# Kernel optimization log

Hardware: AMD Instinct MI355X
Metric: run time of the kernel (lower is better)

The kernel has to match this reference:

```python
import jax, jax.numpy as jnp
import numpy as np

N_NODES = 8192
IN_DIM = 128
HIDDEN = 128
N_EDGES = 262144


def gcn_layer(x, W, b, src, dst, n):
    # GCNConv: h = D^{-1/2}(A+I)D^{-1/2} (x @ W) + b, with added self-loops
    h = x @ W  # [n, out]
    loop = jnp.arange(n, dtype=src.dtype)
    s = jnp.concatenate([src, loop])
    d = jnp.concatenate([dst, loop])
    deg = jax.ops.segment_sum(jnp.ones_like(s, dtype=h.dtype), d, num_segments=n)
    dinv = jax.lax.rsqrt(deg)  # deg >= 1 due to self-loops
    norm = dinv[s] * dinv[d]  # [E+n]
    msg = h[s] * norm[:, None]
    out = jax.ops.segment_sum(msg, d, num_segments=n)
    return out + b


def setup_inputs() -> dict:
    key = jax.random.key(0)
    ks = jax.random.split(key, 10)
    g = 1.0 / np.sqrt(HIDDEN)
    inp = {
        "x": jax.random.normal(ks[0], (N_NODES, IN_DIM), dtype=jnp.float32),
        "edge_index": jax.random.randint(ks[1], (2, N_EDGES), 0, N_NODES, dtype=jnp.int32),
        "W1": jax.random.normal(ks[2], (IN_DIM, HIDDEN), dtype=jnp.float32) * (1.0 / np.sqrt(IN_DIM)),
        "b1": jnp.zeros((HIDDEN,), dtype=jnp.float32),
        "W2": jax.random.normal(ks[3], (HIDDEN, HIDDEN), dtype=jnp.float32) * g,
        "b2": jnp.zeros((HIDDEN,), dtype=jnp.float32),
        "W_out": jax.random.normal(ks[4], (HIDDEN, HIDDEN), dtype=jnp.float32) * g,
        "b_out": jnp.zeros((HIDDEN,), dtype=jnp.float32),
        "W_edge": jax.random.normal(ks[5], (2 * HIDDEN,), dtype=jnp.float32) * (1.0 / np.sqrt(2 * HIDDEN)),
        "b_edge": jnp.zeros((), dtype=jnp.float32),
    }
    return inp


def reference(x, edge_index, W1, b1, W2, b2, W_out, b_out, W_edge, b_edge):
    src, dst = edge_index[0], edge_index[1]
    n = x.shape[0]
    h = jax.nn.relu(gcn_layer(x, W1, b1, src, dst, n))
    h = jax.nn.relu(gcn_layer(h, W2, b2, src, dst, n))
    h = h @ W_out + b_out  # [n, hidden]
    # edge_proj(cat(x_i, x_j)) decomposes: logits[i,j] = h_i.w_i + h_j.w_j + b
    w_i, w_j = W_edge[:HIDDEN], W_edge[HIDDEN:]
    a = h @ w_i  # [n]
    c = h @ w_j  # [n]
    edge_logits = a[:, None] + c[None, :] + b_edge  # [n, n]
    return edge_logits
```

## Files before the change

### kernel.cpp

```cpp
#include <hip/hip_runtime.h>

#define NN 8192
#define NE 262144
#define DIM 128
#define BCAP 128

typedef float f32x4 __attribute__((ext_vector_type(4)));
typedef float f32x2 __attribute__((ext_vector_type(2)));

__device__ __forceinline__ float4 f4fma(float s, float4 w, float4 acc) {
    acc.x = fmaf(s, w.x, acc.x);
    acc.y = fmaf(s, w.y, acc.y);
    acc.z = fmaf(s, w.z, acc.z);
    acc.w = fmaf(s, w.w, acc.w);
    return acc;
}
__device__ __forceinline__ float f4dot(float4 a, float4 b) {
    return fmaf(a.x, b.x, fmaf(a.y, b.y, fmaf(a.z, b.z, a.w * b.w)));
}

__global__ __launch_bounds__(256) void zero_kernel(int* __restrict__ cnt) {
    cnt[blockIdx.x * 256 + threadIdx.x] = 0;
}

__global__ __launch_bounds__(256) void fused_pre(const float* __restrict__ X,
                                                 const float* __restrict__ W,
                                                 float* __restrict__ G,
                                                 const int* __restrict__ src,
                                                 const int* __restrict__ dst,
                                                 int* __restrict__ cnt,
                                                 int* __restrict__ bucket,
                                                 const float* __restrict__ Wout,
                                                 const float* __restrict__ bout,
                                                 const float* __restrict__ we,
                                                 const float* __restrict__ bedge,
                                                 float* __restrict__ u,
                                                 float* __restrict__ v,
                                                 float* __restrict__ beta) {
    __shared__ float4 Wl[128 * 32];
    __shared__ float4 Xl[32 * 32];
    int tid = threadIdx.x;
    int bid = blockIdx.x;

    if (bid < 256) {
        int rbase = bid * 32;
        const float4* W4 = (const float4*)W;
#pragma unroll
        for (int i = 0; i < 16; ++i) Wl[i * 256 + tid] = W4[i * 256 + tid];
        const float4* X4 = (const float4*)(X + rbase * DIM);
#pragma unroll
        for (int i = 0; i < 4; ++i) Xl[i * 256 + tid] = X4[i * 256 + tid];
        __syncthreads();

        int tx = tid & 31;
        int ty = tid >> 5;
        float4 acc[4];
#pragma unroll
        for (int i = 0; i < 4; ++i) acc[i] = make_float4(0.f, 0.f, 0.f, 0.f);

        for (int k4 = 0; k4 < 32; ++k4) {
            float4 w0 = Wl[(k4 * 4 + 0) * 32 + tx];
            float4 w1 = Wl[(k4 * 4 + 1) * 32 + tx];
            float4 w2 = Wl[(k4 * 4 + 2) * 32 + tx];
            float4 w3 = Wl[(k4 * 4 + 3) * 32 + tx];
#pragma unroll
            for (int i = 0; i < 4; ++i) {
                float4 xv = Xl[(ty * 4 + i) * 32 + k4];
                acc[i] = f4fma(xv.x, w0, acc[i]);
                acc[i] = f4fma(xv.y, w1, acc[i]);
                acc[i] = f4fma(xv.z, w2, acc[i]);
                acc[i] = f4fma(xv.w, w3, acc[i]);
            }
        }
        float4* G4 = (float4*)G;
#pragma unroll
        for (int i = 0; i < 4; ++i) {
            int r = rbase + ty * 4 + i;
            G4[r * 32 + tx] = acc[i];
        }
        return;
    }
    if (bid < 1280) {
        int e = (bid - 256) * 256 + tid;
        int d = dst[e];
        int p = atomicAdd(&cnt[d], 1);
        if (p < BCAP) bucket[(d << 7) + p] = src[e];
        return;
    }
    float* red = (float*)Xl;
    int k = tid;
    if (k < DIM) {
        const float4* W4o = (const float4*)(Wout + (k << 7));
        const float4* we4 = (const float4*)we;
        float su = 0.f, sv = 0.f;
#pragma unroll
        for (int j = 0; j < 32; ++j) {
            float4 w = W4o[j];
            su += f4dot(w, we4[j]);
            sv += f4dot(w, we4[32 + j]);
        }
        u[k] = su;
        v[k] = sv;
    }
    red[k] = (k < DIM) ? bout[k] * we[k] : 0.f;
    __syncthreads();
    for (int off = 128; off >= 1; off >>= 1) {
        if (k < off) red[k] += red[k + off];
        __syncthreads();
    }
    float b0 = red[0];
    __syncthreads();
    red[k] = (k < DIM) ? bout[k] * we[DIM + k] : 0.f;
    __syncthreads();
    for (int off = 128; off >= 1; off >>= 1) {
        if (k < off) red[k] += red[k + off];
        __syncthreads();
    }
    if (k == 0) {
        beta[0] = b0 + bedge[0];
        beta[1] = red[0];
    }
}

__global__ __launch_bounds__(256) void gather_scale(const float* __restrict__ G1,
                                                    const int* __restrict__ cnt,
                                                    const int* __restrict__ bucket,
                                                    const float* __restrict__ b1,
                                                    f32x2* __restrict__ S2) {
    int node = blockIdx.x * 4 + (threadIdx.x >> 6);
    int lane = threadIdx.x & 63;
    const float2* G12 = (const float2*)G1;

    int degree = cnt[node];
    float dv = rsqrtf((float)(degree + 1));
    int deg = min(degree, BCAP);
    int i0 = __builtin_nontemporal_load(bucket + (node << 7) + lane);
    int i1 = __builtin_nontemporal_load(bucket + (node << 7) + 64 + lane);

    float2 selfv = G12[node * 64 + lane];
    float ax = selfv.x * dv, ay = selfv.y * dv;
    float px[8], py[8];
#pragma unroll
    for (int k = 0; k < 8; ++k) { px[k] = 0.f; py[k] = 0.f; }

    int d8 = deg & ~7;
    for (int e = 0; e < d8; e += 8) {
        int s[8];
#pragma unroll
        for (int k = 0; k < 8; ++k) s[k] = __shfl((e + k) >= 64 ? i1 : i0, (e + k) & 63);
#pragma unroll
        for (int k = 0; k < 8; ++k) {
            int ck = cnt[s[k]];
            float2 t = G12[s[k] * 64 + lane];
            float w = rsqrtf((float)(ck + 1));
            px[k] = fmaf(t.x, w, px[k]);
            py[k] = fmaf(t.y, w, py[k]);
        }
    }
    for (int e = d8; e < deg; ++e) {
        int s = __shfl(e >= 64 ? i1 : i0, e & 63);
        int ck = cnt[s];
        float2 t = G12[s * 64 + lane];
        float w = rsqrtf((float)(ck + 1));
        ax = fmaf(t.x, w, ax);
        ay = fmaf(t.y, w, ay);
    }
    float yx = ax + ((px[0] + px[1]) + (px[2] + px[3])) + ((px[4] + px[5]) + (px[6] + px[7]));
    float yy = ay + ((py[0] + py[1]) + (py[2] + py[3])) + ((py[4] + py[5]) + (py[6] + py[7]));

    const float2* B2 = (const float2*)b1;
    float2 bb = B2[lane];
    f32x2 o;
    o.x = fmaxf(fmaf(yx, dv, bb.x), 0.f) * dv;
    o.y = fmaxf(fmaf(yy, dv, bb.y), 0.f) * dv;
    __builtin_nontemporal_store(o, S2 + node * 64 + lane);
}

__global__ __launch_bounds__(256) void gemm_mid(const float* __restrict__ X,
                                                const float* __restrict__ W,
                                                float* __restrict__ G) {
    __shared__ float4 Wl[128 * 32];
    __shared__ float4 Xl[32 * 32];
    int tid = threadIdx.x;
    int rbase = blockIdx.x * 32;

    const float4* W4 = (const float4*)W;
#pragma unroll
    for (int i = 0; i < 16; ++i) Wl[i * 256 + tid] = W4[i * 256 + tid];
    const float4* X4 = (const float4*)(X + rbase * DIM);
#pragma unroll
    for (int i = 0; i < 4; ++i) Xl[i * 256 + tid] = X4[i * 256 + tid];
    __syncthreads();

    int tx = tid & 31;
    int ty = tid >> 5;
    float4 acc[4];
#pragma unroll
    for (int i = 0; i < 4; ++i) acc[i] = make_float4(0.f, 0.f, 0.f, 0.f);

    for (int k4 = 0; k4 < 32; ++k4) {
        float4 w0 = Wl[(k4 * 4 + 0) * 32 + tx];
        float4 w1 = Wl[(k4 * 4 + 1) * 32 + tx];
        float4 w2 = Wl[(k4 * 4 + 2) * 32 + tx];
        float4 w3 = Wl[(k4 * 4 + 3) * 32 + tx];
#pragma unroll
        for (int i = 0; i < 4; ++i) {
            float4 xv = Xl[(ty * 4 + i) * 32 + k4];
            acc[i] = f4fma(xv.x, w0, acc[i]);
            acc[i] = f4fma(xv.y, w1, acc[i]);
            acc[i] = f4fma(xv.z, w2, acc[i]);
            acc[i] = f4fma(xv.w, w3, acc[i]);
        }
    }

    float4* G4 = (float4*)G;
#pragma unroll
    for (int i = 0; i < 4; ++i) {
        int r = rbase + ty * 4 + i;
        G4[r * 32 + tx] = acc[i];
    }
}

__global__ __launch_bounds__(256) void agg_head(const float* __restrict__ G2,
                                                const int* __restrict__ cnt,
                                                const int* __restrict__ bucket,
                                                const float* __restrict__ b2,
                                                const float* __restrict__ u,
                                                const float* __restrict__ v,
                                                const float* __restrict__ beta,
                                                float* __restrict__ a,
                                                float* __restrict__ c) {
    int node = blockIdx.x * 4 + (threadIdx.x >> 6);
    int lane = threadIdx.x & 63;
    const float2* G22 = (const float2*)G2;

    int degree = cnt[node];
    float dv = rsqrtf((float)(degree + 1));
    int deg = min(degree, BCAP);
    int i0 = __builtin_nontemporal_load(bucket + (node << 7) + lane);
    int i1 = __builtin_nontemporal_load(bucket + (node << 7) + 64 + lane);

    float2 selfv = G22[node * 64 + lane];
    float ax = selfv.x, ay = selfv.y;
    float px[8], py[8];
#pragma unroll
    for (int k = 0; k < 8; ++k) { px[k] = 0.f; py[k] = 0.f; }

    int d8 = deg & ~7;
    for (int e = 0; e < d8; e += 8) {
        int s[8];
#pragma unroll
        for (int k = 0; k < 8; ++k) s[k] = __shfl((e + k) >= 64 ? i1 : i0, (e + k) & 63);
#pragma unroll
        for (int k = 0; k < 8; ++k) {
            float2 t = G22[s[k] * 64 + lane];
            px[k] += t.x;
            py[k] += t.y;
        }
    }
    for (int e = d8; e < deg; ++e) {
        int s = __shfl(e >= 64 ? i1 : i0, e & 63);
        float2 t = G22[s * 64 + lane];
        ax += t.x;
        ay += t.y;
    }
    float yx = ax + ((px[0] + px[1]) + (px[2] + px[3])) + ((px[4] + px[5]) + (px[6] + px[7]));
    float yy = ay + ((py[0] + py[1]) + (py[2] + py[3])) + ((py[4] + py[5]) + (py[6] + py[7]));

    const float2* B2 = (const float2*)b2;
    float2 bb = B2[lane];
    float h0 = fmaxf(fmaf(yx, dv, bb.x), 0.f);
    float h1 = fmaxf(fmaf(yy, dv, bb.y), 0.f);

    float2 uu = ((const float2*)u)[lane];
    float2 vv = ((const float2*)v)[lane];
    float pa = h0 * uu.x + h1 * uu.y;
    float pc = h0 * vv.x + h1 * vv.y;
#pragma unroll
    for (int off = 32; off >= 1; off >>= 1) {
        pa += __shfl_xor(pa, off);
        pc += __shfl_xor(pc, off);
    }
    if (lane == 0) {
        a[node] = pa + beta[0];
        c[node] = pc + beta[1];
    }
}

__global__ __launch_bounds__(256) void out_kernel(const float* __restrict__ a,
                                                  const float* __restrict__ c,
                                                  f32x4* __restrict__ out) {
    const f32x4* c4 = (const f32x4*)c;
    size_t base = (size_t)blockIdx.x * 1024 + threadIdx.x;
#pragma unroll
    for (int q = 0; q < 4; ++q) {
        size_t idx = base + q * 256;
        int i = (int)(idx >> 11);
        int j4 = (int)(idx & 2047);
        f32x4 r = c4[j4] + a[i];
        out[idx] = r;
    }
}

extern "C" void kernel_launch(void* const* d_in, const int* in_sizes, int n_in,
                              void* d_out, int out_size, void* d_ws, size_t ws_size,
                              hipStream_t stream) {
    const float* x    = (const float*)d_in[0];
    const int*   ei   = (const int*)d_in[1];
    const float* W1   = (const float*)d_in[2];
    const float* b1   = (const float*)d_in[3];
    const float* W2   = (const float*)d_in[4];
    const float* b2   = (const float*)d_in[5];
    const float* Wout = (const float*)d_in[6];
    const float* bout = (const float*)d_in[7];
    const float* We   = (const float*)d_in[8];
    const float* bedge= (const float*)d_in[9];
    const int* src = ei;
    const int* dst = ei + NE;

    int* cnt     = (int*)d_ws;
    int* bucket  = cnt + NN;
    float* u     = (float*)(bucket + NN * BCAP);
    float* v     = u + DIM;
    float* beta  = v + DIM;
    float* g1    = beta + 16;
    float* s2    = g1 + NN * DIM;
    float* g2    = s2 + NN * DIM;
    float* av    = g2 + NN * DIM;
    float* cv    = av + NN;

    float* out = (float*)d_out;

    zero_kernel<<<32, 256, 0, stream>>>(cnt);
    fused_pre<<<1281, 256, 0, stream>>>(x, W1, g1, src, dst, cnt, bucket,
                                        Wout, bout, We, bedge, u, v, beta);
    gather_scale<<<NN / 4, 256, 0, stream>>>(g1, cnt, bucket, b1, (f32x2*)s2);
    gemm_mid<<<NN / 32, 256, 0, stream>>>(s2, W2, g2);
    agg_head<<<NN / 4, 256, 0, stream>>>(g2, cnt, bucket, b2, u, v, beta, av, cv);
    out_kernel<<<(NN * NN / 4) / 1024, 256, 0, stream>>>(av, cv, (f32x4*)out);
}
```

Measured before the change: 110.0 us.

## Build edge buckets with chunked LDS histograms, scan, and deterministic placement

Replaces global-atomic bucket construction with a three-phase counting sort. Each of 64 chunks builds a per-destination histogram in shared memory, a scan kernel computes per-chunk offsets, and a place kernel scatters source indices using LDS atomics. The aim is to remove contention on global atomics and the separate zero kernel. In exchange it adds two kernel launches, a 64x8192 histogram round-trip through memory, and place_kernel runs only 64 blocks, which limits parallelism.

```diff
diff --git a/kernel.cpp b/kernel.cpp
--- a/kernel.cpp
+++ b/kernel.cpp
@@ -4,6 +4,8 @@
 #define NE 262144
 #define DIM 128
 #define BCAP 128
+#define NCH 64
+#define CHE (NE / NCH)
 
 typedef float f32x4 __attribute__((ext_vector_type(4)));
 typedef float f32x2 __attribute__((ext_vector_type(2)));
@@ -19,17 +21,11 @@
     return fmaf(a.x, b.x, fmaf(a.y, b.y, fmaf(a.z, b.z, a.w * b.w)));
 }
 
-__global__ __launch_bounds__(256) void zero_kernel(int* __restrict__ cnt) {
-    cnt[blockIdx.x * 256 + threadIdx.x] = 0;
-}
-
 __global__ __launch_bounds__(256) void fused_pre(const float* __restrict__ X,
                                                  const float* __restrict__ W,
                                                  float* __restrict__ G,
-                                                 const int* __restrict__ src,
                                                  const int* __restrict__ dst,
-                                                 int* __restrict__ cnt,
-                                                 int* __restrict__ bucket,
+                                                 int* __restrict__ hist,
                                                  const float* __restrict__ Wout,
                                                  const float* __restrict__ bout,
                                                  const float* __restrict__ we,
@@ -37,8 +33,10 @@
                                                  float* __restrict__ u,
                                                  float* __restrict__ v,
                                                  float* __restrict__ beta) {
-    __shared__ float4 Wl[128 * 32];
-    __shared__ float4 Xl[32 * 32];
+    __shared__ char smem[80 * 1024] __attribute__((aligned(16)));
+    float4* Wl = (float4*)smem;
+    float4* Xl = (float4*)(smem + 64 * 1024);
+    int* histL = (int*)smem;
     int tid = threadIdx.x;
     int bid = blockIdx.x;
 
@@ -80,11 +78,17 @@
         }
         return;
     }
-    if (bid < 1280) {
-        int e = (bid - 256) * 256 + tid;
-        int d = dst[e];
-        int p = atomicAdd(&cnt[d], 1);
-        if (p < BCAP) bucket[(d << 7) + p] = src[e];
+    if (bid < 256 + NCH) {
+        int c = bid - 256;
+        for (int i = tid; i < NN; i += 256) histL[i] = 0;
+        __syncthreads();
+        const int* dch = dst + c * CHE;
+        for (int i = tid; i < CHE; i += 256) {
+            atomicAdd(&histL[dch[i]], 1);
+        }
+        __syncthreads();
+        int* hc = hist + c * NN;
+        for (int i = tid; i < NN; i += 256) hc[i] = histL[i];
         return;
     }
     float* red = (float*)Xl;
@@ -119,6 +123,39 @@
     if (k == 0) {
         beta[0] = b0 + bedge[0];
         beta[1] = red[0];
+    }
+}
+
+__global__ __launch_bounds__(256) void scan_kernel(const int* __restrict__ hist,
+                                                   int* __restrict__ offs,
+                                                   int* __restrict__ cnt) {
+    int n = blockIdx.x * 256 + threadIdx.x;
+    int run = n << 7;
+#pragma unroll
+    for (int c = 0; c < NCH; ++c) {
+        int t = hist[c * NN + n];
+        offs[c * NN + n] = run;
+        run += t;
+    }
+    cnt[n] = run - (n << 7);
+}
+
+__global__ __launch_bounds__(256) void place_kernel(const int* __restrict__ src,
+                                                    const int* __restrict__ dst,
+                                                    const int* __restrict__ offs,
+                                                    int* __restrict__ bucket) {
+    __shared__ int cur[NN];
+    int tid = threadIdx.x;
+    int c = blockIdx.x;
+    const int* oc = offs + c * NN;
+    for (int i = tid; i < NN; i += 256) cur[i] = oc[i];
+    __syncthreads();
+    const int* sch = src + c * CHE;
+    const int* dch = dst + c * CHE;
+    for (int i = tid; i < CHE; i += 256) {
+        int d = dch[i];
+        int p = atomicAdd(&cur[d], 1);
+        if (p < ((d + 1) << 7)) bucket[p] = sch[i];
     }
 }
 
@@ -328,12 +365,15 @@
     float* g2    = s2 + NN * DIM;
     float* av    = g2 + NN * DIM;
     float* cv    = av + NN;
+    int* hist    = (int*)(cv + NN);
+    int* offs    = hist + NCH * NN;
 
     float* out = (float*)d_out;
 
-    zero_kernel<<<32, 256, 0, stream>>>(cnt);
-    fused_pre<<<1281, 256, 0, stream>>>(x, W1, g1, src, dst, cnt, bucket,
-                                        Wout, bout, We, bedge, u, v, beta);
+    fused_pre<<<256 + NCH + 1, 256, 0, stream>>>(x, W1, g1, dst, hist,
+                                                 Wout, bout, We, bedge, u, v, beta);
+    scan_kernel<<<NN / 256, 256, 0, stream>>>(hist, offs, cnt);
+    place_kernel<<<NCH, 256, 0, stream>>>(src, dst, offs, bucket);
     gather_scale<<<NN / 4, 256, 0, stream>>>(g1, cnt, bucket, b1, (f32x2*)s2);
     gemm_mid<<<NN / 32, 256, 0, stream>>>(s2, W2, g2);
     agg_head<<<NN / 4, 256, 0, stream>>>(g2, cnt, bucket, b2, u, v, beta, av, cv);
```

Measured after the change: 115.1 us. +4.7%, slower.

## Fuse layer-1 neighbor gather with layer-2 GEMM in one kernel

Applied to the files above, without the earlier changes.

Merges the gather_scale aggregation and the gemm_mid matrix multiply into a single kernel. Each wave aggregates 8 nodes and writes the result into shared memory, which then feeds the W2 GEMM directly, removing the s2 round trip through global memory and one launch. Neighbor weights are precomputed per lane and broadcast with shuffles, and the 8 nodes are processed in lockstep up to the maximum degree. The cost is that the grid drops to 256 blocks, shared-memory pressure rises, and the work is padded to the highest degree among each wave's 8 nodes.

```diff
diff --git a/kernel.cpp b/kernel.cpp
--- a/kernel.cpp
+++ b/kernel.cpp
@@ -122,102 +122,103 @@
     }
 }
 
-__global__ __launch_bounds__(256) void gather_scale(const float* __restrict__ G1,
-                                                    const int* __restrict__ cnt,
-                                                    const int* __restrict__ bucket,
-                                                    const float* __restrict__ b1,
-                                                    f32x2* __restrict__ S2) {
-    int node = blockIdx.x * 4 + (threadIdx.x >> 6);
-    int lane = threadIdx.x & 63;
-    const float2* G12 = (const float2*)G1;
-
-    int degree = cnt[node];
-    float dv = rsqrtf((float)(degree + 1));
-    int deg = min(degree, BCAP);
-    int i0 = __builtin_nontemporal_load(bucket + (node << 7) + lane);
-    int i1 = __builtin_nontemporal_load(bucket + (node << 7) + 64 + lane);
-
-    float2 selfv = G12[node * 64 + lane];
-    float ax = selfv.x * dv, ay = selfv.y * dv;
-    float px[8], py[8];
-#pragma unroll
-    for (int k = 0; k < 8; ++k) { px[k] = 0.f; py[k] = 0.f; }
-
-    int d8 = deg & ~7;
-    for (int e = 0; e < d8; e += 8) {
-        int s[8];
-#pragma unroll
-        for (int k = 0; k < 8; ++k) s[k] = __shfl((e + k) >= 64 ? i1 : i0, (e + k) & 63);
-#pragma unroll
-        for (int k = 0; k < 8; ++k) {
-            int ck = cnt[s[k]];
-            float2 t = G12[s[k] * 64 + lane];
-            float w = rsqrtf((float)(ck + 1));
-            px[k] = fmaf(t.x, w, px[k]);
-            py[k] = fmaf(t.y, w, py[k]);
-        }
-    }
-    for (int e = d8; e < deg; ++e) {
-        int s = __shfl(e >= 64 ? i1 : i0, e & 63);
-        int ck = cnt[s];
-        float2 t = G12[s * 64 + lane];
-        float w = rsqrtf((float)(ck + 1));
-        ax = fmaf(t.x, w, ax);
-        ay = fmaf(t.y, w, ay);
-    }
-    float yx = ax + ((px[0] + px[1]) + (px[2] + px[3])) + ((px[4] + px[5]) + (px[6] + px[7]));
-    float yy = ay + ((py[0] + py[1]) + (py[2] + py[3])) + ((py[4] + py[5]) + (py[6] + py[7]));
-
-    const float2* B2 = (const float2*)b1;
-    float2 bb = B2[lane];
-    f32x2 o;
-    o.x = fmaxf(fmaf(yx, dv, bb.x), 0.f) * dv;
-    o.y = fmaxf(fmaf(yy, dv, bb.y), 0.f) * dv;
-    __builtin_nontemporal_store(o, S2 + node * 64 + lane);
-}
-
-__global__ __launch_bounds__(256) void gemm_mid(const float* __restrict__ X,
-                                                const float* __restrict__ W,
-                                                float* __restrict__ G) {
+__global__ __launch_bounds__(256) void gather_gemm(const float* __restrict__ G1,
+                                                   const int* __restrict__ cnt,
+                                                   const int* __restrict__ bucket,
+                                                   const float* __restrict__ b1,
+                                                   const float* __restrict__ W2,
+                                                   float* __restrict__ G2) {
     __shared__ float4 Wl[128 * 32];
     __shared__ float4 Xl[32 * 32];
     int tid = threadIdx.x;
     int rbase = blockIdx.x * 32;
-
-    const float4* W4 = (const float4*)W;
+    int w = tid >> 6;
+    int lane = tid & 63;
+    const float2* G12 = (const float2*)G1;
+
+    int deg[8], i0[8], i1[8];
+    float dv[8], w0[8], w1[8];
+    float2 acc[8];
+    int nb = rbase + w * 8;
+#pragma unroll
+    for (int j = 0; j < 8; ++j) {
+        int n = nb + j;
+        int degree = cnt[n];
+        dv[j] = rsqrtf((float)(degree + 1));
+        deg[j] = min(degree, BCAP);
+        int a0 = __builtin_nontemporal_load(bucket + (n << 7) + lane);
+        int a1 = __builtin_nontemporal_load(bucket + (n << 7) + 64 + lane);
+        i0[j] = (lane < deg[j]) ? a0 : 0;
+        i1[j] = (64 + lane < deg[j]) ? a1 : 0;
+        acc[j] = G12[n * 64 + lane];
+        acc[j].x *= dv[j];
+        acc[j].y *= dv[j];
+    }
+#pragma unroll
+    for (int j = 0; j < 8; ++j) {
+        w0[j] = rsqrtf((float)(cnt[i0[j]] + 1));
+        w1[j] = rsqrtf((float)(cnt[i1[j]] + 1));
+    }
+
+    const float4* W4 = (const float4*)W2;
 #pragma unroll
     for (int i = 0; i < 16; ++i) Wl[i * 256 + tid] = W4[i * 256 + tid];
-    const float4* X4 = (const float4*)(X + rbase * DIM);
-#pragma unroll
-    for (int i = 0; i < 4; ++i) Xl[i * 256 + tid] = X4[i * 256 + tid];
+
+    int m = max(max(max(deg[0], deg[1]), max(deg[2], deg[3])),
+                max(max(deg[4], deg[5]), max(deg[6], deg[7])));
+    for (int e = 0; e < m; ++e) {
+        int lo = e & 63;
+        bool hi = e >= 64;
+#pragma unroll
+        for (int j = 0; j < 8; ++j) {
+            int s = __shfl(hi ? i1[j] : i0[j], lo);
+            float wt = __shfl(hi ? w1[j] : w0[j], lo);
+            bool val = e < deg[j];
+            wt = val ? wt : 0.f;
+            float2 t = G12[s * 64 + lane];
+            acc[j].x = fmaf(t.x, wt, acc[j].x);
+            acc[j].y = fmaf(t.y, wt, acc[j].y);
+        }
+    }
+
+    const float2* B2 = (const float2*)b1;
+    float2 bb = B2[lane];
+    float2* Xl2 = (float2*)Xl;
+#pragma unroll
+    for (int j = 0; j < 8; ++j) {
+        float2 o;
+        o.x = fmaxf(fmaf(acc[j].x, dv[j], bb.x), 0.f) * dv[j];
+        o.y = fmaxf(fmaf(acc[j].y, dv[j], bb.y), 0.f) * dv[j];
+        Xl2[(w * 8 + j) * 64 + lane] = o;
+    }
     __syncthreads();
 
     int tx = tid & 31;
     int ty = tid >> 5;
-    float4 acc[4];
-#pragma unroll
-    for (int i = 0; i < 4; ++i) acc[i] = make_float4(0.f, 0.f, 0.f, 0.f);
+    float4 accg[4];
+#pragma unroll
+    for (int i = 0; i < 4; ++i) accg[i] = make_float4(0.f, 0.f, 0.f, 0.f);
 
     for (int k4 = 0; k4 < 32; ++k4) {
-        float4 w0 = Wl[(k4 * 4 + 0) * 32 + tx];
-        float4 w1 = Wl[(k4 * 4 + 1) * 32 + tx];
-        float4 w2 = Wl[(k4 * 4 + 2) * 32 + tx];
-        float4 w3 = Wl[(k4 * 4 + 3) * 32 + tx];
+        float4 q0 = Wl[(k4 * 4 + 0) * 32 + tx];
+        float4 q1 = Wl[(k4 * 4 + 1) * 32 + tx];
+        float4 q2 = Wl[(k4 * 4 + 2) * 32 + tx];
+        float4 q3 = Wl[(k4 * 4 + 3) * 32 + tx];
 #pragma unroll
         for (int i = 0; i < 4; ++i) {
             float4 xv = Xl[(ty * 4 + i) * 32 + k4];
-            acc[i] = f4fma(xv.x, w0, acc[i]);
-            acc[i] = f4fma(xv.y, w1, acc[i]);
-            acc[i] = f4fma(xv.z, w2, acc[i]);
-            acc[i] = f4fma(xv.w, w3, acc[i]);
-        }
-    }
-
-    float4* G4 = (float4*)G;
+            accg[i] = f4fma(xv.x, q0, accg[i]);
+            accg[i] = f4fma(xv.y, q1, accg[i]);
+            accg[i] = f4fma(xv.z, q2, accg[i]);
+            accg[i] = f4fma(xv.w, q3, accg[i]);
+        }
+    }
+
+    float4* G4 = (float4*)G2;
 #pragma unroll
     for (int i = 0; i < 4; ++i) {
         int r = rbase + ty * 4 + i;
-        G4[r * 32 + tx] = acc[i];
+        G4[r * 32 + tx] = accg[i];
     }
 }
 
@@ -324,8 +325,7 @@
     float* v     = u + DIM;
     float* beta  = v + DIM;
     float* g1    = beta + 16;
-    float* s2    = g1 + NN * DIM;
-    float* g2    = s2 + NN * DIM;
+    float* g2    = g1 + NN * DIM;
     float* av    = g2 + NN * DIM;
     float* cv    = av + NN;
 
@@ -334,8 +334,7 @@
     zero_kernel<<<32, 256, 0, stream>>>(cnt);
     fused_pre<<<1281, 256, 0, stream>>>(x, W1, g1, src, dst, cnt, bucket,
                                         Wout, bout, We, bedge, u, v, beta);
-    gather_scale<<<NN / 4, 256, 0, stream>>>(g1, cnt, bucket, b1, (f32x2*)s2);
-    gemm_mid<<<NN / 32, 256, 0, stream>>>(s2, W2, g2);
+    gather_gemm<<<NN / 32, 256, 0, stream>>>(g1, cnt, bucket, b1, W2, g2);
     agg_head<<<NN / 4, 256, 0, stream>>>(g2, cnt, bucket, b2, u, v, beta, av, cv);
     out_kernel<<<(NN * NN / 4) / 1024, 256, 0, stream>>>(av, cv, (f32x4*)out);
 }
```

Measured after the change: 113.7 us. +3.4%, slower.
